# Kernel optimization log

Measured on AMD Instinct MI355X. Metric: run time of the kernel, lower is better.

The kernel has to match this reference:

```python
import jax, jax.numpy as jnp
import numpy as np

B, D, H = 128, 256, 512  # batch, input_size, hidden_size; 2 hidden layers
ORDER = 'A'
EPS = 1e-12


def _masks():
    # Standard MADE sequential degrees: inputs 1..D (reversed for order 'B'),
    # hidden degrees cycle over 1..D-1. Hidden mask: >=, output mask: > (strict).
    din = np.arange(1, D + 1) if ORDER == 'A' else np.arange(D, 0, -1)
    dh = (np.arange(H) % (D - 1)) + 1
    m0 = (dh[:, None] >= din[None, :]).astype(np.float32)  # [H, D]
    m1 = (dh[:, None] >= dh[None, :]).astype(np.float32)   # [H, H]
    mo = (din[:, None] > dh[None, :]).astype(np.float32)   # [D, H]
    return jnp.asarray(m0), jnp.asarray(m1), jnp.asarray(mo)


def _made(y, W0, b0, W1, b1, Wo, bo, masks):
    m0, m1, mo = masks
    h = jax.nn.elu(y @ (W0 * m0).T + b0)   # [B, H]
    h = jax.nn.elu(h @ (W1 * m1).T + b1)   # [B, H]
    return h @ (Wo * mo).T + bo            # [B, D]


def setup_inputs() -> dict:
    key = jax.random.key(0)
    ks = jax.random.split(key, 13)
    s_in, s_h = 1.0 / np.sqrt(D), 1.0 / np.sqrt(H)

    def p(k, shape, s):
        return (jax.random.normal(k, shape, jnp.float32) * s).astype(jnp.float32)

    return {
        'x': jax.random.normal(ks[0], (B, D), jnp.float32),
        'mu_W0': p(ks[1], (H, D), s_in), 'mu_b0': jnp.zeros((H,), jnp.float32),
        'mu_W1': p(ks[2], (H, H), s_h),  'mu_b1': jnp.zeros((H,), jnp.float32),
        'mu_Wo': p(ks[3], (D, H), s_h),  'mu_bo': jnp.zeros((D,), jnp.float32),
        'lv_W0': p(ks[4], (H, D), s_in), 'lv_b0': jnp.zeros((H,), jnp.float32),
        'lv_W1': p(ks[5], (H, H), s_h),  'lv_b1': jnp.zeros((H,), jnp.float32),
        'lv_Wo': p(ks[6], (D, H), s_h),  'lv_bo': jnp.zeros((D,), jnp.float32),
    }


def reference(x, mu_W0, mu_b0, mu_W1, mu_b1, mu_Wo, mu_bo,
              lv_W0, lv_b0, lv_W1, lv_b1, lv_Wo, lv_bo):
    masks = _masks()
    idx = jnp.arange(D) if ORDER == 'A' else jnp.arange(D - 1, -1, -1)

    def step(carry, i):
        y, _ = carry
        mu = _made(y, mu_W0, mu_b0, mu_W1, mu_b1, mu_Wo, mu_bo, masks)
        logstd = 0.5 * _made(y, lv_W0, lv_b0, lv_W1, lv_b1, lv_Wo, lv_bo, masks)
        new_col = (x[:, i] - mu[:, i]) / (jnp.exp(logstd[:, i]) + EPS)
        y = y.at[:, i].set(new_col)
        return (y, logstd), None

    init = (jnp.zeros_like(x), jnp.zeros_like(x))
    (y, logstd), _ = jax.lax.scan(step, init, idx)
    return y, logstd.sum(axis=1)
```

## Files before the change

kernel.cpp:

```cpp
#include <hip/hip_runtime.h>

#define DD 256
#define HH 512
#define BB 128
#define TS 4096

#define WAITVM(N) asm volatile("s_waitcnt vmcnt(" #N ")" ::: "memory")
#define PIN4(v) asm volatile("" :: "v"((v).x), "v"((v).y), "v"((v).z), "v"((v).w))

__device__ __forceinline__ float elu_f(float x) {
    return x > 0.f ? x : (__expf(x) - 1.f);
}
__device__ __forceinline__ float rlf(float v, int l) {
    return __uint_as_float(__builtin_amdgcn_readlane(__float_as_uint(v), (unsigned)l));
}
__device__ __forceinline__ float f4c(const float4& v, int r) {
    return r == 0 ? v.x : r == 1 ? v.y : r == 2 ? v.z : v.w;
}

__device__ __forceinline__ int pmap(int h) {
    if (h == 510) return 255;
    if (h == 511) return 511;
    return (h < 255) ? (4 * (h & 63) + (h >> 6))
                     : (256 + 4 * ((h - 255) & 63) + ((h - 255) >> 6));
}
__device__ __forceinline__ int p4map(int j) {
    return 4 * (j & 63) + (j >> 6);
}
__device__ __forceinline__ int w1base(int hp) {
    return (hp <= 254) ? hp * TS
         : (hp <= 509) ? (hp - 255) * TS + 1024
         : 255 * TS + ((hp == 510) ? 0 : 1024);
}
__device__ __forceinline__ int wobase(int hp) {
    return (hp <= 254) ? hp * TS + 3072
         : (hp <= 509) ? (hp - 255) * TS + 3584
         : 255 * TS + ((hp == 510) ? 2048 : 2560);
}

__global__ __launch_bounds__(256) void prep(
    const float* __restrict__ w0m_, const float* __restrict__ w0l_,
    const float* __restrict__ w1m_, const float* __restrict__ w1l_,
    const float* __restrict__ wom_, const float* __restrict__ wol_,
    float* __restrict__ tape)
{
    __shared__ float tm[32][33], tl[32][33];
    const int tx = threadIdx.x & 31, ty = threadIdx.x >> 5;
    const unsigned b = blockIdx.x;

    if (b < 256) {
        const int h0 = (int)(b >> 4) << 5, hp0 = (int)(b & 15) << 5;
        #pragma unroll
        for (int j = 0; j < 4; ++j) {
            int r = ty + 8 * j;
            tm[r][tx] = w1m_[(h0 + r) * HH + hp0 + tx];
            tl[r][tx] = w1l_[(h0 + r) * HH + hp0 + tx];
        }
        __syncthreads();
        #pragma unroll
        for (int j = 0; j < 4; ++j) {
            int hp = hp0 + ty + 8 * j;
            int h  = h0 + tx;
            int dh_h = (h <= 254) ? h + 1 : (h <= 509 ? h - 254 : h - 509);
            int dh_p = (hp <= 254) ? hp + 1 : (hp <= 509 ? hp - 254 : hp - 509);
            float mask = (dh_h >= dh_p) ? 1.f : 0.f;
            int base = w1base(hp), p = pmap(h);
            tape[base + p]       = mask * tm[tx][ty + 8 * j];
            tape[base + 512 + p] = mask * tl[tx][ty + 8 * j];
        }
    } else if (b < 384) {
        const int b2 = (int)b - 256;
        const int h0 = (b2 >> 3) << 5, i0 = (b2 & 7) << 5;
        #pragma unroll
        for (int j = 0; j < 4; ++j) {
            int r = ty + 8 * j;
            tm[r][tx] = w0m_[(h0 + r) * DD + i0 + tx];
            tl[r][tx] = w0l_[(h0 + r) * DD + i0 + tx];
        }
        __syncthreads();
        #pragma unroll
        for (int j = 0; j < 4; ++j) {
            int i = i0 + ty + 8 * j;
            int h = h0 + tx;
            int p = pmap(h);
            tape[i * TS + 2048 + p] = tm[tx][ty + 8 * j];
            tape[i * TS + 2560 + p] = tl[tx][ty + 8 * j];
        }
    } else {
        const int b3 = (int)b - 384;
        const int j0 = (b3 >> 4) << 5, hp0 = (b3 & 15) << 5;
        #pragma unroll
        for (int j = 0; j < 4; ++j) {
            int r = ty + 8 * j;
            tm[r][tx] = wom_[(j0 + r) * HH + hp0 + tx];
            tl[r][tx] = wol_[(j0 + r) * HH + hp0 + tx];
        }
        __syncthreads();
        #pragma unroll
        for (int j = 0; j < 4; ++j) {
            int hp = hp0 + ty + 8 * j;
            int jj = j0 + tx;
            int base = wobase(hp), p = p4map(jj);
            tape[base + p]       = tm[tx][ty + 8 * j];
            tape[base + 256 + p] = tl[tx][ty + 8 * j];
        }
    }
}

__device__ __forceinline__ void stage16(const float* g, float* l, int lane) {
    #pragma unroll
    for (int k = 0; k < 16; ++k) {
        __builtin_amdgcn_global_load_lds(
            (const __attribute__((address_space(1))) void*)(g + 256 * k + 4 * lane),
            (__attribute__((address_space(3))) void*)(l + 256 * k),
            16, 0, 0);
    }
}

struct MSet { float4 w8, w9, w0, w4, w1, w5, w12, w14; };
struct LSet { float4 w10, w11, w2, w6, w3, w7, w13, w15; };

__device__ __forceinline__ void rdM(MSet& S, const float* b, int lane) {
    const float4* p = (const float4*)b;
    S.w8  = p[64 * 8 + lane];  S.w9  = p[64 * 9 + lane];
    S.w0  = p[64 * 0 + lane];  S.w4  = p[64 * 4 + lane];
    S.w1  = p[64 * 1 + lane];  S.w5  = p[64 * 5 + lane];
    S.w12 = p[64 * 12 + lane]; S.w14 = p[64 * 14 + lane];
}
__device__ __forceinline__ void rdL(LSet& S, const float* b, int lane) {
    const float4* p = (const float4*)b;
    S.w10 = p[64 * 10 + lane]; S.w11 = p[64 * 11 + lane];
    S.w2  = p[64 * 2 + lane];  S.w6  = p[64 * 6 + lane];
    S.w3  = p[64 * 3 + lane];  S.w7  = p[64 * 7 + lane];
    S.w13 = p[64 * 13 + lane]; S.w15 = p[64 * 15 + lane];
}
__device__ __forceinline__ void pinM(const MSet& S) {
    PIN4(S.w8); PIN4(S.w9); PIN4(S.w0); PIN4(S.w4);
    PIN4(S.w1); PIN4(S.w5); PIN4(S.w12); PIN4(S.w14);
}
__device__ __forceinline__ void pinL(const LSet& S) {
    PIN4(S.w10); PIN4(S.w11); PIN4(S.w2); PIN4(S.w6);
    PIN4(S.w3); PIN4(S.w7); PIN4(S.w13); PIN4(S.w15);
}

template<int Q, int EX>
__device__ __forceinline__ void stepM(
    int tl, int lane, float v, const MSet& S,
    float (&a0m)[8], float (&a1m)[8], float (&Rm)[4], float (&yv)[4],
    const float4& exA, const float4& exB, const float4& exW)
{
    yv[Q] = (lane == tl) ? v : yv[Q];

    #pragma unroll
    for (int r = Q; r < 4; ++r) {
        a0m[r]     += v * f4c(S.w8, r);
        a0m[4 + r] += v * f4c(S.w9, r);
    }
    float p0 = elu_f(rlf(a0m[Q], tl));
    float p1 = elu_f(rlf(a0m[4 + Q], tl));
    float p2 = 0.f;
    if (EX) p2 = elu_f(rlf(a0m[EX == 1 ? 3 : 7], 63));

    #pragma unroll
    for (int r = Q; r < 4; ++r) {
        a1m[r]     += f4c(S.w0, r) * p0 + f4c(S.w4, r) * p1;
        a1m[4 + r] += f4c(S.w1, r) * p0 + f4c(S.w5, r) * p1;
    }
    if (EX) {
        #pragma unroll
        for (int r = 0; r < 4; ++r) {
            a1m[r]     += f4c(exA, r) * p2;
            a1m[4 + r] += f4c(exB, r) * p2;
        }
    }

    float q0 = elu_f(rlf(a1m[Q], tl));
    float q1 = elu_f(rlf(a1m[4 + Q], tl));
    float q2 = 0.f;
    if (EX) q2 = elu_f(rlf(a1m[EX == 1 ? 3 : 7], 63));

    #pragma unroll
    for (int r = Q; r < 4; ++r)
        Rm[r] += f4c(S.w12, r) * q0 + f4c(S.w14, r) * q1;
    if (EX) {
        #pragma unroll
        for (int r = 0; r < 4; ++r) Rm[r] += f4c(exW, r) * q2;
    }
}

template<int Q, int EX>
__device__ __forceinline__ void stepL(
    int tl, int lane, float v, const LSet& S,
    float (&a0l)[8], float (&a1l)[8], float (&Rl)[4],
    const float4& exA, const float4& exB, const float4& exW)
{
    #pragma unroll
    for (int r = Q; r < 4; ++r) {
        a0l[r]     += v * f4c(S.w10, r);
        a0l[4 + r] += v * f4c(S.w11, r);
    }
    float p0 = elu_f(rlf(a0l[Q], tl));
    float p1 = elu_f(rlf(a0l[4 + Q], tl));
    float p2 = 0.f;
    if (EX) p2 = elu_f(rlf(a0l[EX == 1 ? 3 : 7], 63));

    #pragma unroll
    for (int r = Q; r < 4; ++r) {
        a1l[r]     += f4c(S.w2, r) * p0 + f4c(S.w6, r) * p1;
        a1l[4 + r] += f4c(S.w3, r) * p0 + f4c(S.w7, r) * p1;
    }
    if (EX) {
        #pragma unroll
        for (int r = 0; r < 4; ++r) {
            a1l[r]     += f4c(exA, r) * p2;
            a1l[4 + r] += f4c(exB, r) * p2;
        }
    }

    float q0 = elu_f(rlf(a1l[Q], tl));
    float q1 = elu_f(rlf(a1l[4 + Q], tl));
    float q2 = 0.f;
    if (EX) q2 = elu_f(rlf(a1l[EX == 1 ? 3 : 7], 63));

    #pragma unroll
    for (int r = Q; r < 4; ++r)
        Rl[r] += f4c(S.w13, r) * q0 + f4c(S.w15, r) * q1;
    if (EX) {
        #pragma unroll
        for (int r = 0; r < 4; ++r) Rl[r] += f4c(exW, r) * q2;
    }
}

__global__ __launch_bounds__(192, 1) void made_main(
    const float* __restrict__ x,
    const float* __restrict__ mu_b0, const float* __restrict__ mu_b1,
    const float* __restrict__ mu_bo,
    const float* __restrict__ lv_b0, const float* __restrict__ lv_b1,
    const float* __restrict__ lv_bo,
    const float* __restrict__ tape,
    float* __restrict__ out)
{
    __shared__ __align__(16) float buf[4][TS];
    __shared__ __align__(8) float exch[2][2];
    const int row  = blockIdx.x;
    const int lane = threadIdx.x & 63;
    const int wid  = threadIdx.x >> 6;

    const float4 d4 = make_float4(0.f, 0.f, 0.f, 0.f);

    if (wid == 2) {
        #pragma unroll
        for (int g = 0; g < 3; ++g)
            stage16(tape + (size_t)g * TS, &buf[g][0], lane);
        #pragma unroll 1
        for (int t = 0; t < 255; ++t) {
            if (t < 253) { WAITVM(16); } else { WAITVM(0); }
            __builtin_amdgcn_s_barrier();
            __builtin_amdgcn_sched_barrier(0);
            int g = t + 3;
            if (g < 255)
                stage16(tape + (size_t)g * TS, &buf[g & 3][0], lane);
        }
        __builtin_amdgcn_s_barrier();
        return;
    }

    const float4* a4 = (const float4*)(tape + 255 * TS);

    if (wid == 0) {
        float a0m[8], a1m[8], Rm[4], yv[4], xv[4], bmv[4];
        #pragma unroll
        for (int r = 0; r < 4; ++r) {
            a0m[r]     = mu_b0[lane + 64 * r];
            a0m[4 + r] = mu_b0[255 + lane + 64 * r];
            a1m[r]     = mu_b1[lane + 64 * r];
            a1m[4 + r] = mu_b1[255 + lane + 64 * r];
            Rm[r] = 0.f; yv[r] = 0.f;
            xv[r]  = x[row * DD + 64 * r + lane];
            bmv[r] = mu_bo[64 * r + lane];
        }
        if (lane == 63) {
            a0m[3] = mu_b0[510]; a0m[7] = mu_b0[511];
            a1m[3] = mu_b1[510]; a1m[7] = mu_b1[511];
        }
        float4 e510A = a4[lane],       e510B = a4[64 + lane];
        float4 e511A = a4[256 + lane], e511B = a4[320 + lane];
        float4 wo510 = a4[512 + lane], wo511 = a4[640 + lane];

        MSet A, B;

        {
            float d0 = xv[0] - (Rm[0] + bmv[0]);
            if (lane == 0) exch[0][0] = d0;
        }

        __syncthreads();
        {
            float2 ds0 = *(const float2*)&exch[0][0];
            float v0 = ds0.x * ds0.y;
            rdM(A, &buf[0][0], lane);
            rdM(B, &buf[1][0], lane);
            stepM<0, 1>(0, lane, v0, A, a0m, a1m, Rm, yv, e510A, e510B, wo510);
            float dn = xv[0] - (Rm[0] + bmv[0]);
            if (lane == 1) exch[1][0] = dn;
            pinM(B);
        }
        __syncthreads();
        {
            float2 ds1 = *(const float2*)&exch[1][0];
            float v1 = ds1.x * ds1.y;
            rdM(A, &buf[2][0], lane);
            stepM<0, 2>(1, lane, v1, B, a0m, a1m, Rm, yv, e511A, e511B, wo511);
            float dn = xv[0] - (Rm[0] + bmv[0]);
            if (lane == 2) exch[0][0] = dn;
            pinM(A);
        }

#define MBODY(Q, tt, Qn, tn, SC, SN, PREF)                                    \
    {                                                                         \
        __syncthreads();                                                      \
        float2 ds_ = *(const float2*)&exch[(tt) & 1][0];                      \
        float v_ = ds_.x * ds_.y;                                             \
        if (PREF) rdM(SN, &buf[((tt) + 1) & 3][0], lane);                     \
        stepM<Q, 0>((tt) - 64 * (Q), lane, v_, SC, a0m, a1m, Rm, yv,          \
                    d4, d4, d4);                                              \
        float dn_ = xv[Qn] - (Rm[Qn] + bmv[Qn]);                              \
        if (lane == (tn)) exch[((tt) + 1) & 1][0] = dn_;                      \
        if (PREF) pinM(SN);                                                   \
    }
        #pragma unroll 1
        for (int t = 2; t < 62; t += 2) {
            MBODY(0, t, 0, t + 1, A, B, 1)
            MBODY(0, t + 1, 0, t + 2, B, A, 1)
        }
        MBODY(0, 62, 0, 63, A, B, 1)
        MBODY(0, 63, 1, 0, B, A, 1)
        #pragma unroll 1
        for (int t = 64; t < 126; t += 2) {
            MBODY(1, t, 1, t - 63, A, B, 1)
            MBODY(1, t + 1, 1, t - 62, B, A, 1)
        }
        MBODY(1, 126, 1, 63, A, B, 1)
        MBODY(1, 127, 2, 0, B, A, 1)
        #pragma unroll 1
        for (int t = 128; t < 190; t += 2) {
            MBODY(2, t, 2, t - 127, A, B, 1)
            MBODY(2, t + 1, 2, t - 126, B, A, 1)
        }
        MBODY(2, 190, 2, 63, A, B, 1)
        MBODY(2, 191, 3, 0, B, A, 1)
        #pragma unroll 1
        for (int t = 192; t < 252; t += 2) {
            MBODY(3, t, 3, t - 191, A, B, 1)
            MBODY(3, t + 1, 3, t - 190, B, A, 1)
        }
        MBODY(3, 252, 3, 61, A, B, 1)
        MBODY(3, 253, 3, 62, B, A, 1)
        MBODY(3, 254, 3, 63, A, B, 0)
#undef MBODY

        __syncthreads();
        {
            float2 dsF = *(const float2*)&exch[1][0];
            yv[3] = (lane == 63) ? dsF.x * dsF.y : yv[3];
        }
        #pragma unroll
        for (int r = 0; r < 4; ++r) out[row * DD + 64 * r + lane] = yv[r];
    } else {
        float a0l[8], a1l[8], Rl[4], xv[4], blv[4];
        #pragma unroll
        for (int r = 0; r < 4; ++r) {
            a0l[r]     = lv_b0[lane + 64 * r];
            a0l[4 + r] = lv_b0[255 + lane + 64 * r];
            a1l[r]     = lv_b1[lane + 64 * r];
            a1l[4 + r] = lv_b1[255 + lane + 64 * r];
            Rl[r] = 0.f;
            xv[r]  = x[row * DD + 64 * r + lane];
            blv[r] = lv_bo[64 * r + lane];
        }
        if (lane == 63) {
            a0l[3] = lv_b0[510]; a0l[7] = lv_b0[511];
            a1l[3] = lv_b1[510]; a1l[7] = lv_b1[511];
        }
        float4 e510A = a4[128 + lane], e510B = a4[192 + lane];
        float4 e511A = a4[384 + lane], e511B = a4[448 + lane];
        float4 wo510 = a4[576 + lane], wo511 = a4[704 + lane];

        LSet A, B;
        float ls_part = 0.f;

        {
            float ls0 = 0.5f * (Rl[0] + blv[0]);
            float s0  = __fdividef(1.f, __expf(ls0) + 1e-12f);
            ls_part += (lane == 0) ? ls0 : 0.f;
            if (lane == 0) exch[0][1] = s0;
        }

        __syncthreads();
        {
            float2 ds0 = *(const float2*)&exch[0][0];
            float v0 = ds0.x * ds0.y;
            rdL(A, &buf[0][0], lane);
            rdL(B, &buf[1][0], lane);
            stepL<0, 1>(0, lane, v0, A, a0l, a1l, Rl, e510A, e510B, wo510);
            float lsn = 0.5f * (Rl[0] + blv[0]);
            float sn  = __fdividef(1.f, __expf(lsn) + 1e-12f);
            ls_part += (lane == 1) ? lsn : 0.f;
            if (lane == 1) exch[1][1] = sn;
            pinL(B);
        }
        __syncthreads();
        {
            float2 ds1 = *(const float2*)&exch[1][0];
            float v1 = ds1.x * ds1.y;
            rdL(A, &buf[2][0], lane);
            stepL<0, 2>(1, lane, v1, B, a0l, a1l, Rl, e511A, e511B, wo511);
            float lsn = 0.5f * (Rl[0] + blv[0]);
            float sn  = __fdividef(1.f, __expf(lsn) + 1e-12f);
            ls_part += (lane == 2) ? lsn : 0.f;
            if (lane == 2) exch[0][1] = sn;
            pinL(A);
        }

#define LBODY(Q, tt, Qn, tn, SC, SN, PREF)                                    \
    {                                                                         \
        __syncthreads();                                                      \
        float2 ds_ = *(const float2*)&exch[(tt) & 1][0];                      \
        float v_ = ds_.x * ds_.y;                                             \
        if (PREF) rdL(SN, &buf[((tt) + 1) & 3][0], lane);                     \
        stepL<Q, 0>((tt) - 64 * (Q), lane, v_, SC, a0l, a1l, Rl, d4, d4, d4); \
        float lsn_ = 0.5f * (Rl[Qn] + blv[Qn]);                               \
        float sn_  = __fdividef(1.f, __expf(lsn_) + 1e-12f);                  \
        ls_part += (lane == (tn)) ? lsn_ : 0.f;                               \
        if (lane == (tn)) exch[((tt) + 1) & 1][1] = sn_;                      \
        if (PREF) pinL(SN);                                                   \
    }
        #pragma unroll 1
        for (int t = 2; t < 62; t += 2) {
            LBODY(0, t, 0, t + 1, A, B, 1)
            LBODY(0, t + 1, 0, t + 2, B, A, 1)
        }
        LBODY(0, 62, 0, 63, A, B, 1)
        LBODY(0, 63, 1, 0, B, A, 1)
        #pragma unroll 1
        for (int t = 64; t < 126; t += 2) {
            LBODY(1, t, 1, t - 63, A, B, 1)
            LBODY(1, t + 1, 1, t - 62, B, A, 1)
        }
        LBODY(1, 126, 1, 63, A, B, 1)
        LBODY(1, 127, 2, 0, B, A, 1)
        #pragma unroll 1
        for (int t = 128; t < 190; t += 2) {
            LBODY(2, t, 2, t - 127, A, B, 1)
            LBODY(2, t + 1, 2, t - 126, B, A, 1)
        }
        LBODY(2, 190, 2, 63, A, B, 1)
        LBODY(2, 191, 3, 0, B, A, 1)
        #pragma unroll 1
        for (int t = 192; t < 252; t += 2) {
            LBODY(3, t, 3, t - 191, A, B, 1)
            LBODY(3, t + 1, 3, t - 190, B, A, 1)
        }
        LBODY(3, 252, 3, 61, A, B, 1)
        LBODY(3, 253, 3, 62, B, A, 1)
        LBODY(3, 254, 3, 63, A, B, 0)
#undef LBODY

        __syncthreads();
        #pragma unroll
        for (int off = 32; off; off >>= 1)
            ls_part += __shfl_down(ls_part, off);
        if (lane == 0) out[BB * DD + row] = ls_part;
    }
}

extern "C" void kernel_launch(void* const* d_in, const int* in_sizes, int n_in,
                              void* d_out, int out_size, void* d_ws, size_t ws_size,
                              hipStream_t stream) {
    const float* x     = (const float*)d_in[0];
    const float* mu_W0 = (const float*)d_in[1];
    const float* mu_b0 = (const float*)d_in[2];
    const float* mu_W1 = (const float*)d_in[3];
    const float* mu_b1 = (const float*)d_in[4];
    const float* mu_Wo = (const float*)d_in[5];
    const float* mu_bo = (const float*)d_in[6];
    const float* lv_W0 = (const float*)d_in[7];
    const float* lv_b0 = (const float*)d_in[8];
    const float* lv_W1 = (const float*)d_in[9];
    const float* lv_b1 = (const float*)d_in[10];
    const float* lv_Wo = (const float*)d_in[11];
    const float* lv_bo = (const float*)d_in[12];

    float* tape = (float*)d_ws;

    prep<<<512, 256, 0, stream>>>(mu_W0, lv_W0, mu_W1, lv_W1, mu_Wo, lv_Wo, tape);
    made_main<<<BB, 192, 0, stream>>>(x, mu_b0, mu_b1, mu_bo,
                                      lv_b0, lv_b1, lv_bo, tape, (float*)d_out);
}
```

Measured before the change: 153.9 us.

## Remove dedicated loader wave; compute waves stage their own tape rows into LDS

The separate producer wavefront that streamed tape slices into a 4-deep LDS ring is removed, and the block shrinks from 192 to 128 threads. Each compute wave (mu and logvar) now issues async global-to-LDS loads for only the 8 rows it consumes, three steps ahead. Explicit vmcnt/lgkmcnt waits plus a raw s_barrier replace __syncthreads at the end of each step. The aim is to drop the third wave and split the load traffic between the consumers. The risk is that load issue and wait latency now sit on the critical path of the compute waves.

```diff
diff --git a/kernel.cpp b/kernel.cpp
--- a/kernel.cpp
+++ b/kernel.cpp
@@ -6,6 +6,8 @@
 #define TS 4096
 
 #define WAITVM(N) asm volatile("s_waitcnt vmcnt(" #N ")" ::: "memory")
+#define WAITLGKM0() asm volatile("s_waitcnt lgkmcnt(0)" ::: "memory")
+#define SBAR() do { __builtin_amdgcn_s_barrier(); __builtin_amdgcn_sched_barrier(0); } while (0)
 #define PIN4(v) asm volatile("" :: "v"((v).x), "v"((v).y), "v"((v).z), "v"((v).w))
 
 __device__ __forceinline__ float elu_f(float x) {
@@ -107,12 +109,25 @@
     }
 }
 
-__device__ __forceinline__ void stage16(const float* g, float* l, int lane) {
-    #pragma unroll
-    for (int k = 0; k < 16; ++k) {
+__device__ __forceinline__ void stageM8(const float* g, float* l, int lane) {
+    #pragma unroll
+    for (int k = 0; k < 8; ++k) {
+        const int rows[8] = {8, 9, 0, 4, 1, 5, 12, 14};
+        int r = rows[k];
         __builtin_amdgcn_global_load_lds(
-            (const __attribute__((address_space(1))) void*)(g + 256 * k + 4 * lane),
-            (__attribute__((address_space(3))) void*)(l + 256 * k),
+            (const __attribute__((address_space(1))) void*)(g + 256 * r + 4 * lane),
+            (__attribute__((address_space(3))) void*)(l + 256 * r),
+            16, 0, 0);
+    }
+}
+__device__ __forceinline__ void stageL8(const float* g, float* l, int lane) {
+    #pragma unroll
+    for (int k = 0; k < 8; ++k) {
+        const int rows[8] = {10, 11, 2, 6, 3, 7, 13, 15};
+        int r = rows[k];
+        __builtin_amdgcn_global_load_lds(
+            (const __attribute__((address_space(1))) void*)(g + 256 * r + 4 * lane),
+            (__attribute__((address_space(3))) void*)(l + 256 * r),
             16, 0, 0);
     }
 }
@@ -231,7 +246,7 @@
     }
 }
 
-__global__ __launch_bounds__(192, 1) void made_main(
+__global__ __launch_bounds__(128, 1) void made_main(
     const float* __restrict__ x,
     const float* __restrict__ mu_b0, const float* __restrict__ mu_b1,
     const float* __restrict__ mu_bo,
@@ -247,24 +262,6 @@
     const int wid  = threadIdx.x >> 6;
 
     const float4 d4 = make_float4(0.f, 0.f, 0.f, 0.f);
-
-    if (wid == 2) {
-        #pragma unroll
-        for (int g = 0; g < 3; ++g)
-            stage16(tape + (size_t)g * TS, &buf[g][0], lane);
-        #pragma unroll 1
-        for (int t = 0; t < 255; ++t) {
-            if (t < 253) { WAITVM(16); } else { WAITVM(0); }
-            __builtin_amdgcn_s_barrier();
-            __builtin_amdgcn_sched_barrier(0);
-            int g = t + 3;
-            if (g < 255)
-                stage16(tape + (size_t)g * TS, &buf[g & 3][0], lane);
-        }
-        __builtin_amdgcn_s_barrier();
-        return;
-    }
-
     const float4* a4 = (const float4*)(tape + 255 * TS);
 
     if (wid == 0) {
@@ -287,79 +284,95 @@
         float4 e511A = a4[256 + lane], e511B = a4[320 + lane];
         float4 wo510 = a4[512 + lane], wo511 = a4[640 + lane];
 
+        stageM8(tape + 0 * TS, &buf[0][0], lane);
+        stageM8(tape + 1 * TS, &buf[1][0], lane);
+        stageM8(tape + 2 * TS, &buf[2][0], lane);
+
         MSet A, B;
 
         {
             float d0 = xv[0] - (Rm[0] + bmv[0]);
             if (lane == 0) exch[0][0] = d0;
         }
-
-        __syncthreads();
+        WAITVM(8);
+        WAITLGKM0();
+        SBAR();
+
         {
             float2 ds0 = *(const float2*)&exch[0][0];
             float v0 = ds0.x * ds0.y;
             rdM(A, &buf[0][0], lane);
             rdM(B, &buf[1][0], lane);
+            stageM8(tape + 3 * TS, &buf[3][0], lane);
             stepM<0, 1>(0, lane, v0, A, a0m, a1m, Rm, yv, e510A, e510B, wo510);
             float dn = xv[0] - (Rm[0] + bmv[0]);
             if (lane == 1) exch[1][0] = dn;
             pinM(B);
-        }
-        __syncthreads();
+            WAITVM(8);
+            WAITLGKM0();
+            SBAR();
+        }
         {
             float2 ds1 = *(const float2*)&exch[1][0];
             float v1 = ds1.x * ds1.y;
             rdM(A, &buf[2][0], lane);
+            stageM8(tape + 4 * TS, &buf[0][0], lane);
             stepM<0, 2>(1, lane, v1, B, a0m, a1m, Rm, yv, e511A, e511B, wo511);
             float dn = xv[0] - (Rm[0] + bmv[0]);
             if (lane == 2) exch[0][0] = dn;
             pinM(A);
-        }
-
-#define MBODY(Q, tt, Qn, tn, SC, SN, PREF)                                    \
+            WAITVM(8);
+            WAITLGKM0();
+            SBAR();
+        }
+
+#define MBODY(Q, tt, Qn, tn, SC, SN, PREF, STG)                               \
     {                                                                         \
-        __syncthreads();                                                      \
         float2 ds_ = *(const float2*)&exch[(tt) & 1][0];                      \
         float v_ = ds_.x * ds_.y;                                             \
         if (PREF) rdM(SN, &buf[((tt) + 1) & 3][0], lane);                     \
+        if (STG) stageM8(tape + (size_t)((tt) + 3) * TS,                      \
+                         &buf[((tt) + 3) & 3][0], lane);                      \
         stepM<Q, 0>((tt) - 64 * (Q), lane, v_, SC, a0m, a1m, Rm, yv,          \
                     d4, d4, d4);                                              \
         float dn_ = xv[Qn] - (Rm[Qn] + bmv[Qn]);                              \
         if (lane == (tn)) exch[((tt) + 1) & 1][0] = dn_;                      \
         if (PREF) pinM(SN);                                                   \
+        if (STG) { WAITVM(8); } else { WAITVM(0); }                           \
+        WAITLGKM0();                                                          \
+        SBAR();                                                               \
     }
         #pragma unroll 1
         for (int t = 2; t < 62; t += 2) {
-            MBODY(0, t, 0, t + 1, A, B, 1)
-            MBODY(0, t + 1, 0, t + 2, B, A, 1)
-        }
-        MBODY(0, 62, 0, 63, A, B, 1)
-        MBODY(0, 63, 1, 0, B, A, 1)
+            MBODY(0, t, 0, t + 1, A, B, 1, 1)
+            MBODY(0, t + 1, 0, t + 2, B, A, 1, 1)
+        }
+        MBODY(0, 62, 0, 63, A, B, 1, 1)
+        MBODY(0, 63, 1, 0, B, A, 1, 1)
         #pragma unroll 1
         for (int t = 64; t < 126; t += 2) {
-            MBODY(1, t, 1, t - 63, A, B, 1)
-            MBODY(1, t + 1, 1, t - 62, B, A, 1)
-        }
-        MBODY(1, 126, 1, 63, A, B, 1)
-        MBODY(1, 127, 2, 0, B, A, 1)
+            MBODY(1, t, 1, t - 63, A, B, 1, 1)
+            MBODY(1, t + 1, 1, t - 62, B, A, 1, 1)
+        }
+        MBODY(1, 126, 1, 63, A, B, 1, 1)
+        MBODY(1, 127, 2, 0, B, A, 1, 1)
         #pragma unroll 1
         for (int t = 128; t < 190; t += 2) {
-            MBODY(2, t, 2, t - 127, A, B, 1)
-            MBODY(2, t + 1, 2, t - 126, B, A, 1)
-        }
-        MBODY(2, 190, 2, 63, A, B, 1)
-        MBODY(2, 191, 3, 0, B, A, 1)
+            MBODY(2, t, 2, t - 127, A, B, 1, 1)
+            MBODY(2, t + 1, 2, t - 126, B, A, 1, 1)
+        }
+        MBODY(2, 190, 2, 63, A, B, 1, 1)
+        MBODY(2, 191, 3, 0, B, A, 1, 1)
         #pragma unroll 1
         for (int t = 192; t < 252; t += 2) {
-            MBODY(3, t, 3, t - 191, A, B, 1)
-            MBODY(3, t + 1, 3, t - 190, B, A, 1)
-        }
-        MBODY(3, 252, 3, 61, A, B, 1)
-        MBODY(3, 253, 3, 62, B, A, 1)
-        MBODY(3, 254, 3, 63, A, B, 0)
+            MBODY(3, t, 3, t - 191, A, B, 1, 1)
+            MBODY(3, t + 1, 3, t - 190, B, A, 1, 1)
+        }
+        MBODY(3, 252, 3, 61, A, B, 1, 0)
+        MBODY(3, 253, 3, 62, B, A, 1, 0)
+        MBODY(3, 254, 3, 63, A, B, 0, 0)
 #undef MBODY
 
-        __syncthreads();
         {
             float2 dsF = *(const float2*)&exch[1][0];
             yv[3] = (lane == 63) ? dsF.x * dsF.y : yv[3];
@@ -386,6 +399,10 @@
         float4 e511A = a4[384 + lane], e511B = a4[448 + lane];
         float4 wo510 = a4[576 + lane], wo511 = a4[704 + lane];
 
+        stageL8(tape + 0 * TS, &buf[0][0], lane);
+        stageL8(tape + 1 * TS, &buf[1][0], lane);
+        stageL8(tape + 2 * TS, &buf[2][0], lane);
+
         LSet A, B;
         float ls_part = 0.f;
 
@@ -395,78 +412,90 @@
             ls_part += (lane == 0) ? ls0 : 0.f;
             if (lane == 0) exch[0][1] = s0;
         }
-
-        __syncthreads();
+        WAITVM(8);
+        WAITLGKM0();
+        SBAR();
+
         {
             float2 ds0 = *(const float2*)&exch[0][0];
             float v0 = ds0.x * ds0.y;
             rdL(A, &buf[0][0], lane);
             rdL(B, &buf[1][0], lane);
+            stageL8(tape + 3 * TS, &buf[3][0], lane);
             stepL<0, 1>(0, lane, v0, A, a0l, a1l, Rl, e510A, e510B, wo510);
             float lsn = 0.5f * (Rl[0] + blv[0]);
             float sn  = __fdividef(1.f, __expf(lsn) + 1e-12f);
             ls_part += (lane == 1) ? lsn : 0.f;
             if (lane == 1) exch[1][1] = sn;
             pinL(B);
-        }
-        __syncthreads();
+            WAITVM(8);
+            WAITLGKM0();
+            SBAR();
+        }
         {
             float2 ds1 = *(const float2*)&exch[1][0];
             float v1 = ds1.x * ds1.y;
             rdL(A, &buf[2][0], lane);
+            stageL8(tape + 4 * TS, &buf[0][0], lane);
             stepL<0, 2>(1, lane, v1, B, a0l, a1l, Rl, e511A, e511B, wo511);
             float lsn = 0.5f * (Rl[0] + blv[0]);
             float sn  = __fdividef(1.f, __expf(lsn) + 1e-12f);
             ls_part += (lane == 2) ? lsn : 0.f;
             if (lane == 2) exch[0][1] = sn;
             pinL(A);
-        }
-
-#define LBODY(Q, tt, Qn, tn, SC, SN, PREF)                                    \
+            WAITVM(8);
+            WAITLGKM0();
+            SBAR();
+        }
+
+#define LBODY(Q, tt, Qn, tn, SC, SN, PREF, STG)                               \
     {                                                                         \
-        __syncthreads();                                                      \
         float2 ds_ = *(const float2*)&exch[(tt) & 1][0];                      \
         float v_ = ds_.x * ds_.y;                                             \
         if (PREF) rdL(SN, &buf[((tt) + 1) & 3][0], lane);                     \
+        if (STG) stageL8(tape + (size_t)((tt) + 3) * TS,                      \
+                         &buf[((tt) + 3) & 3][0], lane);                      \
         stepL<Q, 0>((tt) - 64 * (Q), lane, v_, SC, a0l, a1l, Rl, d4, d4, d4); \
         float lsn_ = 0.5f * (Rl[Qn] + blv[Qn]);                               \
         float sn_  = __fdividef(1.f, __expf(lsn_) + 1e-12f);                  \
         ls_part += (lane == (tn)) ? lsn_ : 0.f;                               \
         if (lane == (tn)) exch[((tt) + 1) & 1][1] = sn_;                      \
         if (PREF) pinL(SN);                                                   \
+        if (STG) { WAITVM(8); } else { WAITVM(0); }                           \
+        WAITLGKM0();                                                          \
+        SBAR();                                                               \
     }
         #pragma unroll 1
         for (int t = 2; t < 62; t += 2) {
-            LBODY(0, t, 0, t + 1, A, B, 1)
-            LBODY(0, t + 1, 0, t + 2, B, A, 1)
-        }
-        LBODY(0, 62, 0, 63, A, B, 1)
-        LBODY(0, 63, 1, 0, B, A, 1)
+            LBODY(0, t, 0, t + 1, A, B, 1, 1)
+            LBODY(0, t + 1, 0, t + 2, B, A, 1, 1)
+        }
+        LBODY(0, 62, 0, 63, A, B, 1, 1)
+        LBODY(0, 63, 1, 0, B, A, 1, 1)
         #pragma unroll 1
         for (int t = 64; t < 126; t += 2) {
-            LBODY(1, t, 1, t - 63, A, B, 1)
-            LBODY(1, t + 1, 1, t - 62, B, A, 1)
-        }
-        LBODY(1, 126, 1, 63, A, B, 1)
-        LBODY(1, 127, 2, 0, B, A, 1)
+            LBODY(1, t, 1, t - 63, A, B, 1, 1)
+            LBODY(1, t + 1, 1, t - 62, B, A, 1, 1)
+        }
+        LBODY(1, 126, 1, 63, A, B, 1, 1)
+        LBODY(1, 127, 2, 0, B, A, 1, 1)
         #pragma unroll 1
         for (int t = 128; t < 190; t += 2) {
-            LBODY(2, t, 2, t - 127, A, B, 1)
-            LBODY(2, t + 1, 2, t - 126, B, A, 1)
-        }
-        LBODY(2, 190, 2, 63, A, B, 1)
-        LBODY(2, 191, 3, 0, B, A, 1)
+            LBODY(2, t, 2, t - 127, A, B, 1, 1)
+            LBODY(2, t + 1, 2, t - 126, B, A, 1, 1)
+        }
+        LBODY(2, 190, 2, 63, A, B, 1, 1)
+        LBODY(2, 191, 3, 0, B, A, 1, 1)
         #pragma unroll 1
         for (int t = 192; t < 252; t += 2) {
-            LBODY(3, t, 3, t - 191, A, B, 1)
-            LBODY(3, t + 1, 3, t - 190, B, A, 1)
-        }
-        LBODY(3, 252, 3, 61, A, B, 1)
-        LBODY(3, 253, 3, 62, B, A, 1)
-        LBODY(3, 254, 3, 63, A, B, 0)
+            LBODY(3, t, 3, t - 191, A, B, 1, 1)
+            LBODY(3, t + 1, 3, t - 190, B, A, 1, 1)
+        }
+        LBODY(3, 252, 3, 61, A, B, 1, 0)
+        LBODY(3, 253, 3, 62, B, A, 1, 0)
+        LBODY(3, 254, 3, 63, A, B, 0, 0)
 #undef LBODY
 
-        __syncthreads();
         #pragma unroll
         for (int off = 32; off; off >>= 1)
             ls_part += __shfl_down(ls_part, off);
@@ -494,6 +523,6 @@
     float* tape = (float*)d_ws;
 
     prep<<<512, 256, 0, stream>>>(mu_W0, lv_W0, mu_W1, lv_W1, mu_Wo, lv_Wo, tape);
-    made_main<<<BB, 192, 0, stream>>>(x, mu_b0, mu_b1, mu_bo,
+    made_main<<<BB, 128, 0, stream>>>(x, mu_b0, mu_b1, mu_bo,
                                       lv_b0, lv_b1, lv_bo, tape, (float*)d_out);
 }
```

New measurement: 184.5 us. 19.9% more time.
